# Optimization experiments

Measured on AMD Instinct MI355X. Metric: run time of the kernel, lower is better.

Reference implementation:

```python
import jax, jax.numpy as jnp
import numpy as np

H = W = 32
V = 1.5  # gaussian sigma used by the original _gussin(1.5)

def _gaussian_table():
    # gus[p, x, y] with p = i*32 + k, matching the original nested loops.
    r = np.arange(H, dtype=np.float64)
    d = (r[:, None, None, None] - r[None, None, :, None]) ** 2 \
        + (r[None, :, None, None] - r[None, None, None, :]) ** 2  # [i,k,x,y]
    g = np.exp(-d / (2.0 * V * V)) / (2.0 * np.pi * V * V)
    g = g.reshape(H * W, H, W)
    g = g / g.sum(axis=(1, 2), keepdims=True)  # per-position boundary normalization
    return jnp.asarray(g, dtype=jnp.float32)

_GUS = _gaussian_table()  # [1024, 32, 32]

def setup_inputs() -> dict:
    key = jax.random.key(0)
    ks = jax.random.split(key, 5)
    c, r = 1024, 16
    return {
        "x": jax.random.normal(ks[0], (1, c, H, W), jnp.float32),
        "se_w1": jax.random.normal(ks[1], (c // r, c), jnp.float32) * 0.03,
        "se_b1": jnp.zeros((c // r,), jnp.float32),
        "se_w2": jax.random.normal(ks[2], (c, c // r), jnp.float32) * 0.1,
        "se_b2": jnp.zeros((c,), jnp.float32),
        "conv_w": jax.random.normal(ks[3], (c, 2 * c), jnp.float32) * 0.02,
        "bn_gamma": jnp.ones((c,), jnp.float32),
        "bn_beta": jnp.zeros((c,), jnp.float32),
        "bn_mean": jnp.zeros((c,), jnp.float32),
        "bn_var": jnp.ones((c,), jnp.float32),
    }

def reference(x, se_w1, se_b1, se_w2, se_b2, conv_w, bn_gamma, bn_beta, bn_mean, bn_var):
    b, c, h, w = x.shape  # b == 1, h == w == 32 (hardcoded by the gaussian table)
    # ---- SE block ----
    y = x.mean(axis=(2, 3))                              # [b, c]
    y = jax.nn.relu(y @ se_w1.T + se_b1)                 # [b, c//r]
    y = jax.nn.sigmoid(y @ se_w2.T + se_b2)              # [b, c]
    x = x * y[:, :, None, None]
    # ---- gaussian spatial pooling (algebraic form of the O(H^2 W^2 C) expand) ----
    # x_spatial[c, p] = sum_{h,w} x[c,h,w] * gus[p,h,w]
    x_spatial = jnp.einsum('chw,phw->cp', x[0], _GUS).reshape(c, h, w)
    # ---- 3x3 local softmax attention on sigmoid features ----
    xr = jax.nn.sigmoid(x)                               # [1, c, h, w]
    xp = jnp.pad(xr, ((0, 0), (0, 0), (1, 1), (1, 1)))
    # torch F.unfold ordering: feature index = c_idx*9 + kh*3 + kw
    patches = jnp.stack([xp[:, :, i:i + h, j:j + w]
                         for i in range(3) for j in range(3)], axis=2)  # [1, c, 9, h, w]
    u = patches.reshape(c * 9, h * w).T                  # [hw, c*9]
    # faithful to the original reshape(hw, 3, 3, c) (reinterprets the c*9 layout)
    x3 = u.reshape(h * w, 3, 3, c)
    x1 = xr[0].transpose(1, 2, 0).reshape(h * w, 1, 1, c)
    logits = (x1 * x3).sum(-1).reshape(h * w, 9)         # [hw, 9]
    attn = jax.nn.softmax(logits, axis=1).reshape(h * w, 3, 3)
    x_range = jnp.einsum('pij,pijc->cp', attn, x3).reshape(c, h, w)
    # ---- fuse: 1x1 conv (no bias) + eval-mode BatchNorm + ReLU ----
    cat = jnp.concatenate([x_range, x_spatial], axis=0).reshape(b, 2 * c, h, w)
    out = jnp.einsum('oc,bchw->bohw', conv_w, cat)
    inv = jax.lax.rsqrt(bn_var + 1e-5)
    out = (out - bn_mean[None, :, None, None]) * (inv * bn_gamma)[None, :, None, None] \
          + bn_beta[None, :, None, None]
    return jax.nn.relu(out)
```

## Files before the change

kernel.cpp:

```cpp
#include <hip/hip_runtime.h>
#include <hip/hip_bf16.h>


typedef __attribute__((ext_vector_type(8))) short v8s;
typedef __attribute__((ext_vector_type(4))) float v4f;

__device__ __forceinline__ float sigmoidf_(float v) {
    return 1.f / (1.f + __expf(-v));
}
__device__ __forceinline__ unsigned short f2bf(float f) {
    unsigned u = __float_as_uint(f);
    u += 0x7fffu + ((u >> 16) & 1u);
    return (unsigned short)(u >> 16);
}
__device__ __forceinline__ float bf2f(unsigned short s) {
    return __uint_as_float(((unsigned)s) << 16);
}

__global__ __launch_bounds__(256) void k_A(const float* __restrict__ x,
                                           const float* __restrict__ W,
                                           float* __restrict__ mean,
                                           unsigned short* __restrict__ Wb,
                                           unsigned short* __restrict__ K2) {
    __shared__ float Gs[32][32];
    int tid = threadIdx.x, bx = blockIdx.x;
    int wv = tid >> 6, lane = tid & 63;
    {
        int row = tid >> 3, col0 = (tid & 7) << 2;
        float e[4], s = 0.f;
        #pragma unroll
        for (int j = 0; j < 4; ++j) {
            float d = (float)(row - (col0 + j));
            e[j] = __expf(-d * d / 4.5f);
            s += e[j];
        }
        s += __shfl_xor(s, 4, 8);
        s += __shfl_xor(s, 2, 8);
        s += __shfl_xor(s, 1, 8);
        float is = 1.f / s;
        #pragma unroll
        for (int j = 0; j < 4; ++j) Gs[row][col0 + j] = e[j] * is;
    }
    #pragma unroll
    for (int k = 0; k < 8; ++k) {
        int e = (k << 18) + (bx << 10) + (tid << 2);
        float4 v = *(const float4*)(W + e);
        uint2 pk;
        pk.x = (unsigned)f2bf(v.x) | ((unsigned)f2bf(v.y) << 16);
        pk.y = (unsigned)f2bf(v.z) | ((unsigned)f2bf(v.w) << 16);
        *(uint2*)(Wb + e) = pk;
    }
    int c = (bx << 2) + wv;
    const float* xp = x + (size_t)c * 1024;
    float s = 0.f;
    #pragma unroll
    for (int j = 0; j < 4; ++j) {
        float4 v = *(const float4*)(xp + (j << 8) + (lane << 2));
        s += v.x + v.y + v.z + v.w;
    }
    #pragma unroll
    for (int o = 32; o; o >>= 1) s += __shfl_down(s, o);
    if (lane == 0) mean[c] = s * (1.f / 1024.f);
    __syncthreads();
    {
        int p = (bx << 2) + wv;
        float gr = Gs[p >> 5][lane >> 1];
        const float* gq = &Gs[p & 31][(lane & 1) << 4];
        unsigned pk[8];
        #pragma unroll
        for (int t = 0; t < 8; ++t) {
            float v0 = gr * gq[2 * t];
            float v1 = gr * gq[2 * t + 1];
            pk[t] = (unsigned)f2bf(v0) | ((unsigned)f2bf(v1) << 16);
        }
        unsigned short* dst = K2 + (size_t)p * 1024 + (lane << 4);
        *(uint4*)dst = *(uint4*)&pk[0];
        *(uint4*)(dst + 8) = *(uint4*)&pk[4];
    }
}

__global__ __launch_bounds__(1024) void k_se(const float* __restrict__ mean,
                                             const float* __restrict__ w1,
                                             const float* __restrict__ b1,
                                             const float* __restrict__ w2,
                                             const float* __restrict__ b2,
                                             float* __restrict__ y2) {
    __shared__ float ms[1024];
    __shared__ float y1[64];
    __shared__ float w2t[64 * 65];
    int tid = threadIdx.x;
    int c0 = blockIdx.x << 6;
    ms[tid] = mean[tid];
    #pragma unroll
    for (int i = 0; i < 4; ++i) {
        int idx = tid + (i << 10);
        w2t[(idx >> 6) * 65 + (idx & 63)] = w2[(size_t)c0 * 64 + idx];
    }
    __syncthreads();
    int wv = tid >> 6, lane = tid & 63;
    #pragma unroll
    for (int jj = 0; jj < 4; ++jj) {
        int j = (wv << 2) + jj;
        float s = 0.f;
        #pragma unroll
        for (int kk = 0; kk < 4; ++kk) {
            float4 wv4 = *(const float4*)(w1 + (size_t)j * 1024 + kk * 256 + (lane << 2));
            float4 mv  = *(const float4*)&ms[kk * 256 + (lane << 2)];
            s += wv4.x * mv.x + wv4.y * mv.y + wv4.z * mv.z + wv4.w * mv.w;
        }
        #pragma unroll
        for (int o = 32; o; o >>= 1) s += __shfl_down(s, o);
        if (lane == 0) y1[j] = fmaxf(s + b1[j], 0.f);
    }
    __syncthreads();
    int o = tid >> 4, l = tid & 15;
    float s = 0.f;
    #pragma unroll
    for (int jj = 0; jj < 4; ++jj) s += y1[l + (jj << 4)] * w2t[o * 65 + l + (jj << 4)];
    #pragma unroll
    for (int o2 = 8; o2; o2 >>= 1) s += __shfl_down(s, o2, 16);
    if (l == 0) y2[c0 + o] = sigmoidf_(s + b2[c0 + o]);
}

__global__ __launch_bounds__(256) void k_prep(const float* __restrict__ x,
                                              const float* __restrict__ y2,
                                              unsigned short* __restrict__ xrb) {
    __shared__ float T[64][65];
    int tid = threadIdx.x;
    int p0 = blockIdx.x << 6, c0 = blockIdx.y << 6;
    #pragma unroll
    for (int i = 0; i < 4; ++i) {
        int idx = tid + (i << 8);
        int row = idx >> 4;
        int col = (idx & 15) << 2;
        float sc = y2[c0 + row];
        float4 v = *(const float4*)(x + (size_t)(c0 + row) * 1024 + p0 + col);
        T[col + 0][row] = sigmoidf_(v.x * sc);
        T[col + 1][row] = sigmoidf_(v.y * sc);
        T[col + 2][row] = sigmoidf_(v.z * sc);
        T[col + 3][row] = sigmoidf_(v.w * sc);
    }
    __syncthreads();
    #pragma unroll
    for (int i = 0; i < 4; ++i) {
        int idx = tid + (i << 8);
        int prow = idx >> 4;
        int cc = (idx & 15) << 2;
        uint2 pk;
        pk.x = (unsigned)f2bf(T[prow][cc + 0]) | ((unsigned)f2bf(T[prow][cc + 1]) << 16);
        pk.y = (unsigned)f2bf(T[prow][cc + 2]) | ((unsigned)f2bf(T[prow][cc + 3]) << 16);
        *(uint2*)(xrb + (size_t)(p0 + prow) * 1024 + c0 + cc) = pk;
    }
}

union __align__(16) SMem {
    struct { unsigned short As[64 * 72]; unsigned short Bs[64 * 72]; } sp;
    struct { unsigned short val[9216]; float part[9][4]; } at;
};

__global__ __launch_bounds__(256) void k_spattn(const float* __restrict__ x,
                                                const unsigned short* __restrict__ xrb,
                                                const unsigned short* __restrict__ K2,
                                                const float* __restrict__ y2,
                                                unsigned short* __restrict__ Bt) {
    __shared__ SMem sm;
    int tid = threadIdx.x;
    int bx = blockIdx.x;
    int wv = tid >> 6, lane = tid & 63;
    if (bx < 256) {
        int wm = wv & 1, wn = wv >> 1;
        int m0 = (bx >> 4) << 6, n0 = (bx & 15) << 6;
        int col = lane & 15, quad = lane >> 4;
        int smi = tid >> 2;
        int sg = (tid & 3) * 2;
        v4f acc[2][2];
        #pragma unroll
        for (int i = 0; i < 2; ++i)
            #pragma unroll
            for (int j = 0; j < 2; ++j) acc[i][j] = (v4f){0.f, 0.f, 0.f, 0.f};
        const float4* pa = (const float4*)(K2 + (size_t)(m0 + smi) * 1024 + sg * 8);
        const float4* pb = (const float4*)(x + (size_t)(n0 + smi) * 1024 + sg * 8);
        float4 ka0 = pa[0], ka1 = pa[1];
        float4 xa0 = pb[0], xa1 = pb[1], xa2 = pb[2], xa3 = pb[3];
        for (int it = 0; it < 16; ++it) {
            __syncthreads();
            *(float4*)&sm.sp.As[smi * 72 + sg * 8] = ka0;
            *(float4*)&sm.sp.As[smi * 72 + sg * 8 + 8] = ka1;
            uint4 pkb0, pkb1;
            pkb0.x = (unsigned)f2bf(xa0.x) | ((unsigned)f2bf(xa0.y) << 16);
            pkb0.y = (unsigned)f2bf(xa0.z) | ((unsigned)f2bf(xa0.w) << 16);
            pkb0.z = (unsigned)f2bf(xa1.x) | ((unsigned)f2bf(xa1.y) << 16);
            pkb0.w = (unsigned)f2bf(xa1.z) | ((unsigned)f2bf(xa1.w) << 16);
            pkb1.x = (unsigned)f2bf(xa2.x) | ((unsigned)f2bf(xa2.y) << 16);
            pkb1.y = (unsigned)f2bf(xa2.z) | ((unsigned)f2bf(xa2.w) << 16);
            pkb1.z = (unsigned)f2bf(xa3.x) | ((unsigned)f2bf(xa3.y) << 16);
            pkb1.w = (unsigned)f2bf(xa3.z) | ((unsigned)f2bf(xa3.w) << 16);
            *(uint4*)&sm.sp.Bs[smi * 72 + sg * 8] = pkb0;
            *(uint4*)&sm.sp.Bs[smi * 72 + sg * 8 + 8] = pkb1;
            __syncthreads();
            if (it + 1 < 16) {
                int k0 = (it + 1) << 6;
                pa = (const float4*)(K2 + (size_t)(m0 + smi) * 1024 + k0 + sg * 8);
                pb = (const float4*)(x + (size_t)(n0 + smi) * 1024 + k0 + sg * 8);
                ka0 = pa[0]; ka1 = pa[1];
                xa0 = pb[0]; xa1 = pb[1]; xa2 = pb[2]; xa3 = pb[3];
            }
            #pragma unroll
            for (int ks = 0; ks < 2; ++ks) {
                int kg = ks * 4 + quad;
                int rA = wm * 32 + col;
                int rB = wn * 32 + col;
                v8s a0 = *(const v8s*)&sm.sp.As[rA * 72 + kg * 8];
                v8s a1 = *(const v8s*)&sm.sp.As[(rA + 16) * 72 + kg * 8];
                v8s b0 = *(const v8s*)&sm.sp.Bs[rB * 72 + kg * 8];
                v8s b1 = *(const v8s*)&sm.sp.Bs[(rB + 16) * 72 + kg * 8];
                acc[0][0] = __builtin_amdgcn_mfma_f32_16x16x32_bf16(a0, b0, acc[0][0], 0, 0, 0);
                acc[0][1] = __builtin_amdgcn_mfma_f32_16x16x32_bf16(a0, b1, acc[0][1], 0, 0, 0);
                acc[1][0] = __builtin_amdgcn_mfma_f32_16x16x32_bf16(a1, b0, acc[1][0], 0, 0, 0);
                acc[1][1] = __builtin_amdgcn_mfma_f32_16x16x32_bf16(a1, b1, acc[1][1], 0, 0, 0);
            }
        }
        #pragma unroll
        for (int mi = 0; mi < 2; ++mi)
            #pragma unroll
            for (int ni = 0; ni < 2; ++ni) {
                int mb = m0 + wm * 32 + mi * 16 + quad * 4;
                int nn = n0 + wn * 32 + ni * 16 + col;
                float yv = y2[nn];
                #pragma unroll
                for (int r = 0; r < 4; ++r)
                    Bt[(size_t)(mb + r) * 2048 + 1024 + nn] = f2bf(acc[mi][ni][r] * yv);
            }
    } else {
        int p = bx - 256;
        int h = p >> 5, w = p & 31;
        #pragma unroll
        for (int rem = 0; rem < 9; ++rem) {
            int dh = rem / 3 - 1, dw = rem % 3 - 1;
            bool ok = ((unsigned)(h + dh) < 32u) && ((unsigned)(w + dw) < 32u);
            const unsigned short* rp = xrb + (size_t)((h + dh) * 32 + (w + dw)) * 1024;
            #pragma unroll
            for (int j = 0; j < 4; ++j) {
                int cf = tid + (j << 8);
                sm.at.val[cf * 9 + rem] = ok ? rp[cf] : (unsigned short)0;
            }
        }
        __syncthreads();
        float ctr[4], vvq[9][4], lg[9];
        #pragma unroll
        for (int j = 0; j < 4; ++j) ctr[j] = bf2f(sm.at.val[(4 * tid + j) * 9 + 4]);
        #pragma unroll
        for (int q = 0; q < 9; ++q) {
            uint2 pk = *(const uint2*)&sm.at.val[(q << 10) + 4 * tid];
            vvq[q][0] = bf2f((unsigned short)(pk.x & 0xffffu));
            vvq[q][1] = bf2f((unsigned short)(pk.x >> 16));
            vvq[q][2] = bf2f((unsigned short)(pk.y & 0xffffu));
            vvq[q][3] = bf2f((unsigned short)(pk.y >> 16));
            lg[q] = ctr[0] * vvq[q][0] + ctr[1] * vvq[q][1]
                  + ctr[2] * vvq[q][2] + ctr[3] * vvq[q][3];
        }
        #pragma unroll
        for (int q = 0; q < 9; ++q) {
            float s = lg[q];
            #pragma unroll
            for (int o = 32; o; o >>= 1) s += __shfl_down(s, o);
            if (lane == 0) sm.at.part[q][wv] = s;
        }
        __syncthreads();
        float a9[9], mx = -3.4e38f;
        #pragma unroll
        for (int q = 0; q < 9; ++q) {
            a9[q] = sm.at.part[q][0] + sm.at.part[q][1] + sm.at.part[q][2] + sm.at.part[q][3];
            mx = fmaxf(mx, a9[q]);
        }
        float se = 0.f;
        #pragma unroll
        for (int q = 0; q < 9; ++q) { a9[q] = __expf(a9[q] - mx); se += a9[q]; }
        float inv = 1.f / se;
        float o4[4] = {0.f, 0.f, 0.f, 0.f};
        #pragma unroll
        for (int q = 0; q < 9; ++q) {
            float a = a9[q] * inv;
            #pragma unroll
            for (int j = 0; j < 4; ++j) o4[j] += a * vvq[q][j];
        }
        uint2 pk;
        pk.x = (unsigned)f2bf(o4[0]) | ((unsigned)f2bf(o4[1]) << 16);
        pk.y = (unsigned)f2bf(o4[2]) | ((unsigned)f2bf(o4[3]) << 16);
        *(uint2*)(Bt + (size_t)p * 2048 + 4 * tid) = pk;
    }
}

__global__ __launch_bounds__(256) void k_main(
    const unsigned short* __restrict__ A, const unsigned short* __restrict__ B,
    float* __restrict__ outF,
    const float* __restrict__ gamma, const float* __restrict__ beta,
    const float* __restrict__ mu, const float* __restrict__ var) {
    __shared__ unsigned short As[2][64 * 72];
    __shared__ unsigned short Bs[2][64 * 72];
    const int K = 2048;
    int tid = threadIdx.x;
    int wv = tid >> 6, lane = tid & 63;
    int wm = wv & 1, wn = wv >> 1;
    int m0 = blockIdx.y << 6, n0 = blockIdx.x << 6;
    int col = lane & 15, quad = lane >> 4;
    int sm = tid >> 2;
    int sg = (tid & 3) * 2;
    v4f acc[2][2];
    #pragma unroll
    for (int i = 0; i < 2; ++i)
        #pragma unroll
        for (int j = 0; j < 2; ++j) acc[i][j] = (v4f){0.f, 0.f, 0.f, 0.f};

    const float4* pa = (const float4*)(A + (size_t)(m0 + sm) * K + sg * 8);
    const float4* pb = (const float4*)(B + (size_t)(n0 + sm) * K + sg * 8);
    float4 ra0 = pa[0], ra1 = pa[1], rb0 = pb[0], rb1 = pb[1];
    *(float4*)&As[0][sm * 72 + sg * 8] = ra0;
    *(float4*)&As[0][sm * 72 + sg * 8 + 8] = ra1;
    *(float4*)&Bs[0][sm * 72 + sg * 8] = rb0;
    *(float4*)&Bs[0][sm * 72 + sg * 8 + 8] = rb1;
    for (int it = 0; it < 32; ++it) {
        __syncthreads();
        int cur = it & 1;
        if (it + 1 < 32) {
            int k0 = (it + 1) << 6;
            pa = (const float4*)(A + (size_t)(m0 + sm) * K + k0 + sg * 8);
            pb = (const float4*)(B + (size_t)(n0 + sm) * K + k0 + sg * 8);
            ra0 = pa[0]; ra1 = pa[1];
            rb0 = pb[0]; rb1 = pb[1];
        }
        #pragma unroll
        for (int ks = 0; ks < 2; ++ks) {
            int kg = ks * 4 + quad;
            int rA = wm * 32 + col;
            int rB = wn * 32 + col;
            v8s a0 = *(const v8s*)&As[cur][rA * 72 + kg * 8];
            v8s a1 = *(const v8s*)&As[cur][(rA + 16) * 72 + kg * 8];
            v8s b0 = *(const v8s*)&Bs[cur][rB * 72 + kg * 8];
            v8s b1 = *(const v8s*)&Bs[cur][(rB + 16) * 72 + kg * 8];
            acc[0][0] = __builtin_amdgcn_mfma_f32_16x16x32_bf16(a0, b0, acc[0][0], 0, 0, 0);
            acc[0][1] = __builtin_amdgcn_mfma_f32_16x16x32_bf16(a0, b1, acc[0][1], 0, 0, 0);
            acc[1][0] = __builtin_amdgcn_mfma_f32_16x16x32_bf16(a1, b0, acc[1][0], 0, 0, 0);
            acc[1][1] = __builtin_amdgcn_mfma_f32_16x16x32_bf16(a1, b1, acc[1][1], 0, 0, 0);
        }
        if (it + 1 < 32) {
            int nxt = cur ^ 1;
            *(float4*)&As[nxt][sm * 72 + sg * 8] = ra0;
            *(float4*)&As[nxt][sm * 72 + sg * 8 + 8] = ra1;
            *(float4*)&Bs[nxt][sm * 72 + sg * 8] = rb0;
            *(float4*)&Bs[nxt][sm * 72 + sg * 8 + 8] = rb1;
        }
    }
    #pragma unroll
    for (int mi = 0; mi < 2; ++mi)
        #pragma unroll
        for (int ni = 0; ni < 2; ++ni) {
            int mb = m0 + wm * 32 + mi * 16 + quad * 4;
            int nn = n0 + wn * 32 + ni * 16 + col;
            #pragma unroll
            for (int r = 0; r < 4; ++r) {
                int mm = mb + r;
                float iv = rsqrtf(var[mm] + 1e-5f);
                float sc = iv * gamma[mm];
                float sh = beta[mm] - mu[mm] * sc;
                outF[((size_t)mm << 10) + nn] = fmaxf(fmaf(acc[mi][ni][r], sc, sh), 0.f);
            }
        }
}

extern "C" void kernel_launch(void* const* d_in, const int* in_sizes, int n_in,
                              void* d_out, int out_size, void* d_ws, size_t ws_size,
                              hipStream_t stream) {
    const float* x     = (const float*)d_in[0];
    const float* w1    = (const float*)d_in[1];
    const float* b1    = (const float*)d_in[2];
    const float* w2    = (const float*)d_in[3];
    const float* b2    = (const float*)d_in[4];
    const float* cw    = (const float*)d_in[5];
    const float* gamma = (const float*)d_in[6];
    const float* beta  = (const float*)d_in[7];
    const float* mu    = (const float*)d_in[8];
    const float* var   = (const float*)d_in[9];
    float* wsf = (float*)d_ws;
    unsigned short* Wb  = (unsigned short*)wsf;
    unsigned short* Bt  = (unsigned short*)(wsf + (1 << 20));
    unsigned short* xrb = (unsigned short*)(wsf + (2 << 20));
    unsigned short* K2  = (unsigned short*)(wsf + (2 << 20) + (1 << 19));
    float* mean = wsf + (3 << 20);
    float* y2   = mean + 1024;
    float* out  = (float*)d_out;

    dim3 g16(16, 16);
    k_A     <<<256, 256, 0, stream>>>(x, cw, mean, Wb, K2);
    k_se    <<<16, 1024, 0, stream>>>(mean, w1, b1, w2, b2, y2);
    k_prep  <<<g16, 256, 0, stream>>>(x, y2, xrb);
    k_spattn<<<1280, 256, 0, stream>>>(x, xrb, K2, y2, Bt);
    k_main  <<<g16, 256, 0, stream>>>(Wb, Bt, out, gamma, beta, mu, var);
}
```

Measured before the change: 129.5 us.

## Fuse SE into prep, precast x to bf16, widen main GEMM to 512 threads

The SE MLP is folded into k_prep, and each block recomputes the small FC layers redundantly, which removes one kernel launch. k_A now also writes a bf16 copy of x, so k_spattn loads half the bytes and no longer converts in its inner loop. k_main goes to 512 threads with 8 waves of 16x32 tiles to raise occupancy and parallelism. The cost is redundant SE compute across 256 blocks, an extra bf16 write of x, and fewer MFMAs per wave for each LDS load.

```diff
diff --git a/kernel.cpp b/kernel.cpp
--- a/kernel.cpp
+++ b/kernel.cpp
@@ -21,7 +21,8 @@
                                            const float* __restrict__ W,
                                            float* __restrict__ mean,
                                            unsigned short* __restrict__ Wb,
-                                           unsigned short* __restrict__ K2) {
+                                           unsigned short* __restrict__ K2,
+                                           unsigned short* __restrict__ xb) {
     __shared__ float Gs[32][32];
     int tid = threadIdx.x, bx = blockIdx.x;
     int wv = tid >> 6, lane = tid & 63;
@@ -52,15 +53,23 @@
     }
     int c = (bx << 2) + wv;
     const float* xp = x + (size_t)c * 1024;
+    float4 vj[4];
     float s = 0.f;
     #pragma unroll
     for (int j = 0; j < 4; ++j) {
-        float4 v = *(const float4*)(xp + (j << 8) + (lane << 2));
-        s += v.x + v.y + v.z + v.w;
+        vj[j] = *(const float4*)(xp + (j << 8) + (lane << 2));
+        s += vj[j].x + vj[j].y + vj[j].z + vj[j].w;
     }
     #pragma unroll
     for (int o = 32; o; o >>= 1) s += __shfl_down(s, o);
     if (lane == 0) mean[c] = s * (1.f / 1024.f);
+    #pragma unroll
+    for (int j = 0; j < 4; ++j) {
+        uint2 pk;
+        pk.x = (unsigned)f2bf(vj[j].x) | ((unsigned)f2bf(vj[j].y) << 16);
+        pk.y = (unsigned)f2bf(vj[j].z) | ((unsigned)f2bf(vj[j].w) << 16);
+        *(uint2*)(xb + (size_t)c * 1024 + (j << 8) + (lane << 2)) = pk;
+    }
     __syncthreads();
     {
         int p = (bx << 2) + wv;
@@ -79,28 +88,26 @@
     }
 }
 
-__global__ __launch_bounds__(1024) void k_se(const float* __restrict__ mean,
-                                             const float* __restrict__ w1,
-                                             const float* __restrict__ b1,
-                                             const float* __restrict__ w2,
-                                             const float* __restrict__ b2,
-                                             float* __restrict__ y2) {
+__global__ __launch_bounds__(256) void k_prep(const float* __restrict__ x,
+                                              const float* __restrict__ mean,
+                                              const float* __restrict__ w1,
+                                              const float* __restrict__ b1,
+                                              const float* __restrict__ w2,
+                                              const float* __restrict__ b2,
+                                              unsigned short* __restrict__ xrb,
+                                              float* __restrict__ y2out) {
     __shared__ float ms[1024];
-    __shared__ float y1[64];
-    __shared__ float w2t[64 * 65];
+    __shared__ float y1s[64];
+    __shared__ float y2s[64];
+    __shared__ float T[64][65];
     int tid = threadIdx.x;
-    int c0 = blockIdx.x << 6;
-    ms[tid] = mean[tid];
-    #pragma unroll
-    for (int i = 0; i < 4; ++i) {
-        int idx = tid + (i << 10);
-        w2t[(idx >> 6) * 65 + (idx & 63)] = w2[(size_t)c0 * 64 + idx];
-    }
+    int p0 = blockIdx.x << 6, c0 = blockIdx.y << 6;
+    *(float4*)&ms[tid << 2] = *(const float4*)(mean + (tid << 2));
     __syncthreads();
     int wv = tid >> 6, lane = tid & 63;
     #pragma unroll
-    for (int jj = 0; jj < 4; ++jj) {
-        int j = (wv << 2) + jj;
+    for (int jj = 0; jj < 16; ++jj) {
+        int j = (wv << 4) + jj;
         float s = 0.f;
         #pragma unroll
         for (int kk = 0; kk < 4; ++kk) {
@@ -110,30 +117,31 @@
         }
         #pragma unroll
         for (int o = 32; o; o >>= 1) s += __shfl_down(s, o);
-        if (lane == 0) y1[j] = fmaxf(s + b1[j], 0.f);
-    }
-    __syncthreads();
-    int o = tid >> 4, l = tid & 15;
-    float s = 0.f;
-    #pragma unroll
-    for (int jj = 0; jj < 4; ++jj) s += y1[l + (jj << 4)] * w2t[o * 65 + l + (jj << 4)];
-    #pragma unroll
-    for (int o2 = 8; o2; o2 >>= 1) s += __shfl_down(s, o2, 16);
-    if (l == 0) y2[c0 + o] = sigmoidf_(s + b2[c0 + o]);
-}
-
-__global__ __launch_bounds__(256) void k_prep(const float* __restrict__ x,
-                                              const float* __restrict__ y2,
-                                              unsigned short* __restrict__ xrb) {
-    __shared__ float T[64][65];
-    int tid = threadIdx.x;
-    int p0 = blockIdx.x << 6, c0 = blockIdx.y << 6;
+        if (lane == 0) y1s[j] = fmaxf(s + b1[j], 0.f);
+    }
+    __syncthreads();
+    {
+        int ci = tid >> 2, sub = tid & 3;
+        float s = 0.f;
+        const float* w2r = w2 + (size_t)(c0 + ci) * 64 + sub * 16;
+        #pragma unroll
+        for (int i = 0; i < 4; ++i) {
+            float4 wv4 = *(const float4*)(w2r + (i << 2));
+            float4 yv4 = *(const float4*)&y1s[sub * 16 + (i << 2)];
+            s += wv4.x * yv4.x + wv4.y * yv4.y + wv4.z * yv4.z + wv4.w * yv4.w;
+        }
+        s += __shfl_down(s, 2, 4);
+        s += __shfl_down(s, 1, 4);
+        if (sub == 0) y2s[ci] = sigmoidf_(s + b2[c0 + ci]);
+    }
+    __syncthreads();
+    if (blockIdx.x == 0 && tid < 64) y2out[c0 + tid] = y2s[tid];
     #pragma unroll
     for (int i = 0; i < 4; ++i) {
         int idx = tid + (i << 8);
         int row = idx >> 4;
         int col = (idx & 15) << 2;
-        float sc = y2[c0 + row];
+        float sc = y2s[row];
         float4 v = *(const float4*)(x + (size_t)(c0 + row) * 1024 + p0 + col);
         T[col + 0][row] = sigmoidf_(v.x * sc);
         T[col + 1][row] = sigmoidf_(v.y * sc);
@@ -158,7 +166,7 @@
     struct { unsigned short val[9216]; float part[9][4]; } at;
 };
 
-__global__ __launch_bounds__(256) void k_spattn(const float* __restrict__ x,
+__global__ __launch_bounds__(256) void k_spattn(const unsigned short* __restrict__ xb,
                                                 const unsigned short* __restrict__ xrb,
                                                 const unsigned short* __restrict__ K2,
                                                 const float* __restrict__ y2,
@@ -179,31 +187,22 @@
             #pragma unroll
             for (int j = 0; j < 2; ++j) acc[i][j] = (v4f){0.f, 0.f, 0.f, 0.f};
         const float4* pa = (const float4*)(K2 + (size_t)(m0 + smi) * 1024 + sg * 8);
-        const float4* pb = (const float4*)(x + (size_t)(n0 + smi) * 1024 + sg * 8);
+        const float4* pb = (const float4*)(xb + (size_t)(n0 + smi) * 1024 + sg * 8);
         float4 ka0 = pa[0], ka1 = pa[1];
-        float4 xa0 = pb[0], xa1 = pb[1], xa2 = pb[2], xa3 = pb[3];
+        float4 kb0 = pb[0], kb1 = pb[1];
         for (int it = 0; it < 16; ++it) {
             __syncthreads();
             *(float4*)&sm.sp.As[smi * 72 + sg * 8] = ka0;
             *(float4*)&sm.sp.As[smi * 72 + sg * 8 + 8] = ka1;
-            uint4 pkb0, pkb1;
-            pkb0.x = (unsigned)f2bf(xa0.x) | ((unsigned)f2bf(xa0.y) << 16);
-            pkb0.y = (unsigned)f2bf(xa0.z) | ((unsigned)f2bf(xa0.w) << 16);
-            pkb0.z = (unsigned)f2bf(xa1.x) | ((unsigned)f2bf(xa1.y) << 16);
-            pkb0.w = (unsigned)f2bf(xa1.z) | ((unsigned)f2bf(xa1.w) << 16);
-            pkb1.x = (unsigned)f2bf(xa2.x) | ((unsigned)f2bf(xa2.y) << 16);
-            pkb1.y = (unsigned)f2bf(xa2.z) | ((unsigned)f2bf(xa2.w) << 16);
-            pkb1.z = (unsigned)f2bf(xa3.x) | ((unsigned)f2bf(xa3.y) << 16);
-            pkb1.w = (unsigned)f2bf(xa3.z) | ((unsigned)f2bf(xa3.w) << 16);
-            *(uint4*)&sm.sp.Bs[smi * 72 + sg * 8] = pkb0;
-            *(uint4*)&sm.sp.Bs[smi * 72 + sg * 8 + 8] = pkb1;
+            *(float4*)&sm.sp.Bs[smi * 72 + sg * 8] = kb0;
+            *(float4*)&sm.sp.Bs[smi * 72 + sg * 8 + 8] = kb1;
             __syncthreads();
             if (it + 1 < 16) {
                 int k0 = (it + 1) << 6;
                 pa = (const float4*)(K2 + (size_t)(m0 + smi) * 1024 + k0 + sg * 8);
-                pb = (const float4*)(x + (size_t)(n0 + smi) * 1024 + k0 + sg * 8);
+                pb = (const float4*)(xb + (size_t)(n0 + smi) * 1024 + k0 + sg * 8);
                 ka0 = pa[0]; ka1 = pa[1];
-                xa0 = pb[0]; xa1 = pb[1]; xa2 = pb[2]; xa3 = pb[3];
+                kb0 = pb[0]; kb1 = pb[1];
             }
             #pragma unroll
             for (int ks = 0; ks < 2; ++ks) {
@@ -291,7 +290,7 @@
     }
 }
 
-__global__ __launch_bounds__(256) void k_main(
+__global__ __launch_bounds__(512) void k_main(
     const unsigned short* __restrict__ A, const unsigned short* __restrict__ B,
     float* __restrict__ outF,
     const float* __restrict__ gamma, const float* __restrict__ beta,
@@ -301,71 +300,59 @@
     const int K = 2048;
     int tid = threadIdx.x;
     int wv = tid >> 6, lane = tid & 63;
-    int wm = wv & 1, wn = wv >> 1;
+    int wm = wv & 3, wn = wv >> 2;
     int m0 = blockIdx.y << 6, n0 = blockIdx.x << 6;
     int col = lane & 15, quad = lane >> 4;
-    int sm = tid >> 2;
-    int sg = (tid & 3) * 2;
-    v4f acc[2][2];
-    #pragma unroll
-    for (int i = 0; i < 2; ++i)
-        #pragma unroll
-        for (int j = 0; j < 2; ++j) acc[i][j] = (v4f){0.f, 0.f, 0.f, 0.f};
-
-    const float4* pa = (const float4*)(A + (size_t)(m0 + sm) * K + sg * 8);
-    const float4* pb = (const float4*)(B + (size_t)(n0 + sm) * K + sg * 8);
-    float4 ra0 = pa[0], ra1 = pa[1], rb0 = pb[0], rb1 = pb[1];
-    *(float4*)&As[0][sm * 72 + sg * 8] = ra0;
-    *(float4*)&As[0][sm * 72 + sg * 8 + 8] = ra1;
-    *(float4*)&Bs[0][sm * 72 + sg * 8] = rb0;
-    *(float4*)&Bs[0][sm * 72 + sg * 8 + 8] = rb1;
+    int srow = tid >> 3;
+    int schunk = tid & 7;
+    v4f acc[2];
+    acc[0] = (v4f){0.f, 0.f, 0.f, 0.f};
+    acc[1] = (v4f){0.f, 0.f, 0.f, 0.f};
+
+    const float4* pa = (const float4*)(A + (size_t)(m0 + srow) * K + schunk * 8);
+    const float4* pb = (const float4*)(B + (size_t)(n0 + srow) * K + schunk * 8);
+    float4 ra = pa[0], rb = pb[0];
+    *(float4*)&As[0][srow * 72 + schunk * 8] = ra;
+    *(float4*)&Bs[0][srow * 72 + schunk * 8] = rb;
     for (int it = 0; it < 32; ++it) {
         __syncthreads();
         int cur = it & 1;
         if (it + 1 < 32) {
             int k0 = (it + 1) << 6;
-            pa = (const float4*)(A + (size_t)(m0 + sm) * K + k0 + sg * 8);
-            pb = (const float4*)(B + (size_t)(n0 + sm) * K + k0 + sg * 8);
-            ra0 = pa[0]; ra1 = pa[1];
-            rb0 = pb[0]; rb1 = pb[1];
+            pa = (const float4*)(A + (size_t)(m0 + srow) * K + k0 + schunk * 8);
+            pb = (const float4*)(B + (size_t)(n0 + srow) * K + k0 + schunk * 8);
+            ra = pa[0]; rb = pb[0];
         }
         #pragma unroll
         for (int ks = 0; ks < 2; ++ks) {
             int kg = ks * 4 + quad;
-            int rA = wm * 32 + col;
+            int rA = wm * 16 + col;
             int rB = wn * 32 + col;
-            v8s a0 = *(const v8s*)&As[cur][rA * 72 + kg * 8];
-            v8s a1 = *(const v8s*)&As[cur][(rA + 16) * 72 + kg * 8];
+            v8s a  = *(const v8s*)&As[cur][rA * 72 + kg * 8];
             v8s b0 = *(const v8s*)&Bs[cur][rB * 72 + kg * 8];
             v8s b1 = *(const v8s*)&Bs[cur][(rB + 16) * 72 + kg * 8];
-            acc[0][0] = __builtin_amdgcn_mfma_f32_16x16x32_bf16(a0, b0, acc[0][0], 0, 0, 0);
-            acc[0][1] = __builtin_amdgcn_mfma_f32_16x16x32_bf16(a0, b1, acc[0][1], 0, 0, 0);
-            acc[1][0] = __builtin_amdgcn_mfma_f32_16x16x32_bf16(a1, b0, acc[1][0], 0, 0, 0);
-            acc[1][1] = __builtin_amdgcn_mfma_f32_16x16x32_bf16(a1, b1, acc[1][1], 0, 0, 0);
+            acc[0] = __builtin_amdgcn_mfma_f32_16x16x32_bf16(a, b0, acc[0], 0, 0, 0);
+            acc[1] = __builtin_amdgcn_mfma_f32_16x16x32_bf16(a, b1, acc[1], 0, 0, 0);
         }
         if (it + 1 < 32) {
             int nxt = cur ^ 1;
-            *(float4*)&As[nxt][sm * 72 + sg * 8] = ra0;
-            *(float4*)&As[nxt][sm * 72 + sg * 8 + 8] = ra1;
-            *(float4*)&Bs[nxt][sm * 72 + sg * 8] = rb0;
-            *(float4*)&Bs[nxt][sm * 72 + sg * 8 + 8] = rb1;
-        }
-    }
-    #pragma unroll
-    for (int mi = 0; mi < 2; ++mi)
-        #pragma unroll
-        for (int ni = 0; ni < 2; ++ni) {
-            int mb = m0 + wm * 32 + mi * 16 + quad * 4;
-            int nn = n0 + wn * 32 + ni * 16 + col;
-            #pragma unroll
-            for (int r = 0; r < 4; ++r) {
-                int mm = mb + r;
-                float iv = rsqrtf(var[mm] + 1e-5f);
-                float sc = iv * gamma[mm];
-                float sh = beta[mm] - mu[mm] * sc;
-                outF[((size_t)mm << 10) + nn] = fmaxf(fmaf(acc[mi][ni][r], sc, sh), 0.f);
-            }
-        }
+            *(float4*)&As[nxt][srow * 72 + schunk * 8] = ra;
+            *(float4*)&Bs[nxt][srow * 72 + schunk * 8] = rb;
+        }
+    }
+    #pragma unroll
+    for (int ni = 0; ni < 2; ++ni) {
+        int mb = m0 + wm * 16 + quad * 4;
+        int nn = n0 + wn * 32 + ni * 16 + col;
+        #pragma unroll
+        for (int r = 0; r < 4; ++r) {
+            int mm = mb + r;
+            float iv = rsqrtf(var[mm] + 1e-5f);
+            float sc = iv * gamma[mm];
+            float sh = beta[mm] - mu[mm] * sc;
+            outF[((size_t)mm << 10) + nn] = fmaxf(fmaf(acc[ni][r], sc, sh), 0.f);
+        }
+    }
 }
 
 extern "C" void kernel_launch(void* const* d_in, const int* in_sizes, int n_in,
@@ -388,12 +375,12 @@
     unsigned short* K2  = (unsigned short*)(wsf + (2 << 20) + (1 << 19));
     float* mean = wsf + (3 << 20);
     float* y2   = mean + 1024;
+    unsigned short* xb = (unsigned short*)(y2 + 1024);
     float* out  = (float*)d_out;
 
     dim3 g16(16, 16);
-    k_A     <<<256, 256, 0, stream>>>(x, cw, mean, Wb, K2);
-    k_se    <<<16, 1024, 0, stream>>>(mean, w1, b1, w2, b2, y2);
-    k_prep  <<<g16, 256, 0, stream>>>(x, y2, xrb);
-    k_spattn<<<1280, 256, 0, stream>>>(x, xrb, K2, y2, Bt);
-    k_main  <<<g16, 256, 0, stream>>>(Wb, Bt, out, gamma, beta, mu, var);
-}
+    k_A     <<<256, 256, 0, stream>>>(x, cw, mean, Wb, K2, xb);
+    k_prep  <<<g16, 256, 0, stream>>>(x, mean, w1, b1, w2, b2, xrb, y2);
+    k_spattn<<<1280, 256, 0, stream>>>(xb, xrb, K2, y2, Bt);
+    k_main  <<<g16, 512, 0, stream>>>(Wb, Bt, out, gamma, beta, mu, var);
+}
```

New measurement: 129.7 us. About the same (+0.2%).
